# Optimization experiments

Measured on AMD Instinct MI355X. Metric: run time of the kernel, lower is better.

Reference implementation:

```python
import jax, jax.numpy as jnp
import numpy as np
from jax import lax

DILATIONS = (1, 3, 9, 9, 3, 1)  # six mid blocks after the 1x1 input conv


def bilinear_sample(fm, verts):
    # fm: [B,H,W,C]; verts: [B,N,2] in [-1,1]; axis 0 of verts maps to H, axis 1 to W.
    # Matches jax.scipy.ndimage.map_coordinates(order=1, mode='constant'):
    # each out-of-bounds corner contributes 0.
    B, H, W, C = fm.shape
    scale = jnp.array([H - 1, W - 1], fm.dtype) / 2.0
    coords = (verts + 1.0) * scale  # [B,N,2]
    vy, vx = coords[..., 0], coords[..., 1]
    y0 = jnp.floor(vy)
    x0 = jnp.floor(vx)
    wy = (vy - y0)[..., None]
    wx = (vx - x0)[..., None]
    y0i = y0.astype(jnp.int32)
    x0i = x0.astype(jnp.int32)
    fm_flat = fm.reshape(B, H * W, C)

    def corner(yi, xi):
        valid = (yi >= 0) & (yi < H) & (xi >= 0) & (xi < W)
        idx = jnp.clip(yi, 0, H - 1) * W + jnp.clip(xi, 0, W - 1)  # [B,N]
        vals = jnp.take_along_axis(fm_flat, idx[..., None], axis=1)  # [B,N,C]
        return jnp.where(valid[..., None], vals, jnp.zeros((), fm.dtype))

    return ((1 - wy) * (1 - wx) * corner(y0i, x0i)
            + (1 - wy) * wx * corner(y0i, x0i + 1)
            + wy * (1 - wx) * corner(y0i + 1, x0i)
            + wy * wx * corner(y0i + 1, x0i + 1))


def conv1d(x, w, b, dil):
    # x: [B,N,Cin], w: [K,Cin,Cout]; flax nnx.Conv default: stride 1, SAME padding.
    out = lax.conv_general_dilated(x, w, (1,), 'SAME', rhs_dilation=(dil,),
                                   dimension_numbers=('NWC', 'WIO', 'NWC'))
    return out if b is None else out + b


def setup_inputs() -> dict:
    key = jax.random.key(0)
    ks = jax.random.split(key, 8)
    B, N, H, W, Cf, Ch = 16, 1024, 256, 256, 126, 512
    D = Cf + 2
    vertices = jax.random.uniform(ks[0], (B, N, 2), jnp.float32, -1.0, 1.0)
    feature_map = jax.random.normal(ks[1], (B, H, W, Cf), jnp.float32)
    w0 = jax.random.normal(ks[2], (1, D, Ch), jnp.float32) / np.float32(np.sqrt(D))
    b0 = jnp.zeros((Ch,), jnp.float32)
    ws = jax.random.normal(ks[3], (6, 3, Ch, Ch), jnp.float32) / np.float32(np.sqrt(3 * Ch))
    bs = jnp.zeros((6, Ch), jnp.float32)
    w_off = jax.random.normal(ks[4], (1, Ch, 2), jnp.float32) / np.float32(np.sqrt(Ch))
    return {"vertices": vertices, "feature_map": feature_map,
            "w0": w0, "b0": b0, "ws": ws, "bs": bs, "w_off": w_off}


def reference(vertices, feature_map, w0, b0, ws, bs, w_off):
    feat = bilinear_sample(feature_map, vertices)          # [B,N,Cf]
    x = jnp.concatenate([feat, vertices], axis=-1)         # [B,N,Cf+2]
    x = jax.nn.relu(conv1d(x, w0, b0, 1))                  # 1x1 input conv
    for i, dil in enumerate(DILATIONS):                    # fixed 6-layer stack
        x = jax.nn.relu(conv1d(x, ws[i], bs[i], dil))
    return conv1d(x, w_off, None, 1)                       # [B,N,2] offsets
```

## Files before the change

kernel.cpp:

```cpp
#include <hip/hip_runtime.h>

typedef __attribute__((ext_vector_type(4))) float f32x4;
typedef __attribute__((ext_vector_type(8))) _Float16 f16x8;

#define BM 128
#define BK 64

#define OFF_W0T 0
#define OFF_WT  131072
#define OFF_X0  (OFF_WT + 6*512*1536*2)
#define OFF_Y0  (OFF_X0 + 16384*128*2)
#define OFF_Y1  (OFF_Y0 + 16*1056*512*2)

__device__ __forceinline__ void load_lds16(const void* g, void* s) {
    __builtin_amdgcn_global_load_lds(
        (const __attribute__((address_space(1))) void*)g,
        (__attribute__((address_space(3))) void*)s, 16, 0, 0);
}

template<int N> struct IC { static constexpr int v = N; };

__global__ __launch_bounds__(256)
void wprep(const float* __restrict__ ws, const float* __restrict__ w0,
           _Float16* __restrict__ wt, _Float16* __restrict__ w0t)
{
    __shared__ float t[64][65];
    const int tid = threadIdx.x;
    const int tr = tid >> 6;
    const int tc = tid & 63;
    const int z = blockIdx.z;
    if (z < 18) {
        const int l = z / 3, tp = z % 3;
        const float* src = ws + (size_t)z * 512 * 512;
        const int ci0 = blockIdx.y * 64, co0 = blockIdx.x * 64;
        #pragma unroll
        for (int i = 0; i < 16; ++i) { int r = i*4 + tr; t[r][tc] = src[(ci0 + r)*512 + co0 + tc]; }
        __syncthreads();
        _Float16* dst = wt + (size_t)l * 512 * 1536;
        #pragma unroll
        for (int i = 0; i < 16; ++i) { int r = i*4 + tr; dst[(co0 + r)*1536 + tp*512 + ci0 + tc] = (_Float16)t[tc][r]; }
    } else {
        if (blockIdx.y >= 2) return;
        const int ci0 = blockIdx.y * 64, co0 = blockIdx.x * 64;
        #pragma unroll
        for (int i = 0; i < 16; ++i) { int r = i*4 + tr; t[r][tc] = w0[(ci0 + r)*512 + co0 + tc]; }
        __syncthreads();
        #pragma unroll
        for (int i = 0; i < 16; ++i) { int r = i*4 + tr; w0t[(co0 + r)*128 + ci0 + tc] = (_Float16)t[tc][r]; }
    }
}

__global__ __launch_bounds__(256)
void sample_pad_kernel(const float* __restrict__ verts, const float* __restrict__ fm,
                       _Float16* __restrict__ X0, _Float16* __restrict__ Y0,
                       _Float16* __restrict__ Y1)
{
    if (blockIdx.x < 1024) {
        const int i = blockIdx.x * 256 + threadIdx.x;
        const unsigned c2   = i & 255;
        const unsigned t2   = ((unsigned)i) >> 8;
        const unsigned prow = t2 & 31;
        const unsigned b    = (t2 >> 5) & 15;
        const unsigned buf  = t2 >> 9;
        const unsigned row  = prow < 16 ? prow : (1024 + prow);
        unsigned* p = (unsigned*)(buf ? Y1 : Y0);
        p[((size_t)b * 1056 + row) * 256 + c2] = 0u;
        return;
    }
    const int p = (blockIdx.x - 1024) * 4 + (threadIdx.x >> 6);
    const int lane = threadIdx.x & 63;
    const int b = p >> 10;
    const float vy = verts[p*2], vx = verts[p*2 + 1];
    const float cy = (vy + 1.f) * 127.5f;
    const float cx = (vx + 1.f) * 127.5f;
    const float fy = floorf(cy), fx = floorf(cx);
    const int y0 = (int)fy, x0 = (int)fx;
    const float wy = cy - fy, wx = cx - fx;
    float w00 = (1.f - wy) * (1.f - wx), w01 = (1.f - wy) * wx;
    float w10 = wy * (1.f - wx),         w11 = wy * wx;
    const bool vy0 = (unsigned)y0 < 256u, vy1 = (unsigned)(y0 + 1) < 256u;
    const bool vx0 = (unsigned)x0 < 256u, vx1 = (unsigned)(x0 + 1) < 256u;
    w00 = (vy0 && vx0) ? w00 : 0.f;
    w01 = (vy0 && vx1) ? w01 : 0.f;
    w10 = (vy1 && vx0) ? w10 : 0.f;
    w11 = (vy1 && vx1) ? w11 : 0.f;
    const int yc0 = min(max(y0, 0), 255), yc1 = min(max(y0 + 1, 0), 255);
    const int xc0 = min(max(x0, 0), 255), xc1 = min(max(x0 + 1, 0), 255);
    const float* base = fm + (size_t)b * (256 * 256 * 126);
    const float* p00 = base + (yc0 * 256 + xc0) * 126;
    const float* p01 = base + (yc0 * 256 + xc1) * 126;
    const float* p10 = base + (yc1 * 256 + xc0) * 126;
    const float* p11 = base + (yc1 * 256 + xc1) * 126;
    _Float16* xr = X0 + (size_t)p * 128;
    for (int c = lane; c < 126; c += 64) {
        float a = w00 * p00[c] + w01 * p01[c] + w10 * p10[c] + w11 * p11[c];
        xr[c] = (_Float16)a;
    }
    if (lane < 2) xr[126 + lane] = (_Float16)(lane ? vx : vy);
}

__global__ __launch_bounds__(256, 2)
void conv_gemm0(const _Float16* __restrict__ A, const _Float16* __restrict__ WT,
                const float* __restrict__ bias, _Float16* __restrict__ Out)
{
    __shared__ _Float16 Ald[2][128 * 64];
    __shared__ _Float16 Bld[2][128 * 64];
    const int tid  = threadIdx.x;
    const int wid  = tid >> 6;
    const int lane = tid & 63;
    const int wm   = wid >> 1, wn = wid & 1;
    const int b    = blockIdx.x >> 3;
    const int n0   = (blockIdx.x & 7) * 128;
    const int co0  = blockIdx.y * 128;

    const _Float16* Ab = A + ((size_t)b * 1024 + n0) * 128;

    const int srow = lane >> 3;
    const int scol = (((lane & 7) ^ (lane >> 3)) << 3);

    f32x4 acc[4][4] = {};

    #pragma unroll
    for (int ks = 0; ks < 2; ++ks) {
        #pragma unroll
        for (int c = 0; c < 4; ++c) {
            const int grow = 8 * (wid + 4 * c) + srow;
            load_lds16(Ab + (size_t)grow * 128 + ks * 64 + scol, &Ald[ks][(8 * (wid + 4 * c)) * 64]);
        }
        #pragma unroll
        for (int c = 0; c < 4; ++c) {
            const int grow = 8 * (wid + 4 * c) + srow;
            load_lds16(WT + (size_t)(co0 + grow) * 128 + ks * 64 + scol, &Bld[ks][(8 * (wid + 4 * c)) * 64]);
        }
    }

    #pragma unroll
    for (int ks = 0; ks < 2; ++ks) {
        __builtin_amdgcn_sched_barrier(0);
        if (ks == 0) asm volatile("s_waitcnt vmcnt(8)" ::: "memory");
        else         asm volatile("s_waitcnt vmcnt(0)" ::: "memory");
        __builtin_amdgcn_s_barrier();
        __builtin_amdgcn_sched_barrier(0);

        f16x8 af[4][2], bfr[4][2];
        #pragma unroll
        for (int f = 0; f < 4; ++f) {
            const int arow = wm * 64 + f * 16 + (lane & 15);
            const int brow = wn * 64 + f * 16 + (lane & 15);
            #pragma unroll
            for (int kf = 0; kf < 2; ++kf) {
                af[f][kf]  = *(const f16x8*)&Ald[ks][arow * 64 + ((kf * 4 + (lane >> 4)) ^ (arow & 7)) * 8];
                bfr[f][kf] = *(const f16x8*)&Bld[ks][brow * 64 + ((kf * 4 + (lane >> 4)) ^ (brow & 7)) * 8];
            }
        }
        #pragma unroll
        for (int m = 0; m < 4; ++m)
            #pragma unroll
            for (int n = 0; n < 4; ++n)
                #pragma unroll
                for (int kf = 0; kf < 2; ++kf)
                    acc[m][n] = __builtin_amdgcn_mfma_f32_16x16x32_f16(af[m][kf], bfr[n][kf], acc[m][n], 0, 0, 0);
    }

    _Float16* Ob = Out + (size_t)b * (1056 * 512) + (size_t)n0 * 512;
    #pragma unroll
    for (int n = 0; n < 4; ++n) {
        const int co = co0 + wn * 64 + n * 16 + (lane & 15);
        const float bv = bias[co];
        #pragma unroll
        for (int m = 0; m < 4; ++m) {
            #pragma unroll
            for (int j = 0; j < 4; ++j) {
                const int row = wm * 64 + m * 16 + (lane >> 4) * 4 + j;
                float v = acc[m][n][j] + bv;
                v = fmaxf(v, 0.f);
                Ob[(size_t)row * 512 + co] = (_Float16)v;
            }
        }
    }
}

#define ACH_ELEMS (320 * 64)
#define BBUF_ELEMS (128 * 64)
__global__ __launch_bounds__(512, 2)
void conv_gemm8(const _Float16* __restrict__ A, const _Float16* __restrict__ WT,
                const float* __restrict__ bias, _Float16* __restrict__ Out, int dil)
{
    extern __shared__ _Float16 smem[];
    _Float16* Ald = smem;
    _Float16* Bld = smem + 2 * ACH_ELEMS;

    const int tid  = threadIdx.x;
    const int wid  = tid >> 6;
    const int lane = tid & 63;
    const int wm   = wid >> 1;
    const int wn   = wid & 1;

    const int orig = blockIdx.x;
    const int swz  = (orig & 7) * 32 + (orig >> 3);
    const int nblk = swz & 3;
    const int mblk = swz >> 2;
    const int b     = mblk >> 2;
    const int n0row = (mblk & 3) * 256;
    const int co0   = nblk * 128;

    const _Float16* Ab = A + (size_t)b * (1056 * 512) + (size_t)n0row * 512;

    const int srow = lane >> 3;
    const int scol = (((lane & 7) ^ (lane >> 3)) << 3);

    f32x4 acc[4][4] = {};

    auto stageA1 = [&](int cn, int i) {
        const int rb = 8 * (wid + 8 * i);
        const _Float16* src = Ab + (long)(rb + srow - 32) * 512 + cn * 64 + scol;
        load_lds16(src, Ald + (cn & 1) * ACH_ELEMS + rb * 64);
    };
    auto stageB1 = [&](int c2, int t2, int cc) {
        const int grow = 64 * cc + 8 * wid + srow;
        const _Float16* src = WT + (size_t)(co0 + grow) * 1536 + (t2 * 512 + c2 * 64) + scol;
        load_lds16(src, Bld + t2 * BBUF_ELEMS + (64 * cc + 8 * wid) * 64);
    };

    stageA1(0, 0); stageA1(0, 1); stageA1(0, 2); stageA1(0, 3); stageA1(0, 4);
    stageB1(0, 0, 0); stageB1(0, 0, 1);
    stageB1(0, 1, 0); stageB1(0, 1, 1);

    auto body = [&](auto TAPc, auto DOAc, int c) {
        constexpr int TAP = decltype(TAPc)::v;
        constexpr int DOA = decltype(DOAc)::v;

        __builtin_amdgcn_sched_barrier(0);
        if constexpr (TAP == 1 && DOA)       asm volatile("s_waitcnt vmcnt(7)" ::: "memory");
        else if constexpr (TAP == 2 && !DOA) asm volatile("s_waitcnt vmcnt(0)" ::: "memory");
        else                                 asm volatile("s_waitcnt vmcnt(2)" ::: "memory");
        __builtin_amdgcn_s_barrier();
        __builtin_amdgcn_sched_barrier(0);

        const _Float16* Abuf = Ald + (c & 1) * ACH_ELEMS;
        const _Float16* Bbuf = Bld + TAP * BBUF_ELEMS;
        const int shift = (TAP - 1) * dil;
        const int rbase = 32 + wm * 64 + (lane & 15) + shift;
        const int akey  = rbase & 7;
        const int bkey  = lane & 7;

        f16x8 bfr[4][2], af[4][2];
        #pragma unroll
        for (int nf = 0; nf < 4; ++nf) {
            const int row = wn * 64 + nf * 16 + (lane & 15);
            #pragma unroll
            for (int kf = 0; kf < 2; ++kf) {
                const int slot = (kf * 4 + (lane >> 4)) ^ bkey;
                bfr[nf][kf] = *(const f16x8*)&Bbuf[row * 64 + slot * 8];
            }
        }
        #pragma unroll
        for (int kf = 0; kf < 2; ++kf) {
            const int slot = (kf * 4 + (lane >> 4)) ^ akey;
            af[0][kf] = *(const f16x8*)&Abuf[rbase * 64 + slot * 8];
        }
        #pragma unroll
        for (int nf = 0; nf < 4; ++nf)
            #pragma unroll
            for (int kf = 0; kf < 2; ++kf)
                acc[0][nf] = __builtin_amdgcn_mfma_f32_16x16x32_f16(af[0][kf], bfr[nf][kf], acc[0][nf], 0, 0, 0);
        #pragma unroll
        for (int kf = 0; kf < 2; ++kf) {
            const int slot = (kf * 4 + (lane >> 4)) ^ akey;
            af[1][kf] = *(const f16x8*)&Abuf[(rbase + 16) * 64 + slot * 8];
        }
        if constexpr (TAP == 0 && DOA) {
            stageA1(c + 1, 0); stageA1(c + 1, 1); stageA1(c + 1, 2); stageA1(c + 1, 3);
        } else if constexpr (TAP == 0) {
            stageB1(7, 2, 0);
        } else if constexpr (DOA) {
            if constexpr (TAP == 1) stageB1(c + 1, 0, 0);
            else                    stageB1(c + 1, 1, 0);
        }
        #pragma unroll
        for (int nf = 0; nf < 4; ++nf)
            #pragma unroll
            for (int kf = 0; kf < 2; ++kf)
                acc[1][nf] = __builtin_amdgcn_mfma_f32_16x16x32_f16(af[1][kf], bfr[nf][kf], acc[1][nf], 0, 0, 0);
        #pragma unroll
        for (int kf = 0; kf < 2; ++kf) {
            const int slot = (kf * 4 + (lane >> 4)) ^ akey;
            af[2][kf] = *(const f16x8*)&Abuf[(rbase + 32) * 64 + slot * 8];
        }
        if constexpr (TAP == 0 && DOA) {
            stageA1(c + 1, 4);
            stageB1(c, 2, 0); stageB1(c, 2, 1);
        } else if constexpr (TAP == 0) {
            stageB1(7, 2, 1);
        } else if constexpr (DOA) {
            if constexpr (TAP == 1) stageB1(c + 1, 0, 1);
            else                    stageB1(c + 1, 1, 1);
        }
        #pragma unroll
        for (int nf = 0; nf < 4; ++nf)
            #pragma unroll
            for (int kf = 0; kf < 2; ++kf)
                acc[2][nf] = __builtin_amdgcn_mfma_f32_16x16x32_f16(af[2][kf], bfr[nf][kf], acc[2][nf], 0, 0, 0);
        #pragma unroll
        for (int kf = 0; kf < 2; ++kf) {
            const int slot = (kf * 4 + (lane >> 4)) ^ akey;
            af[3][kf] = *(const f16x8*)&Abuf[(rbase + 48) * 64 + slot * 8];
        }
        #pragma unroll
        for (int nf = 0; nf < 4; ++nf)
            #pragma unroll
            for (int kf = 0; kf < 2; ++kf)
                acc[3][nf] = __builtin_amdgcn_mfma_f32_16x16x32_f16(af[3][kf], bfr[nf][kf], acc[3][nf], 0, 0, 0);

        if constexpr (DOA) {
            if constexpr (TAP == 0) {
                __builtin_amdgcn_sched_group_barrier(0x100, 10, 0);
                __builtin_amdgcn_sched_group_barrier(0x008,  8, 0);
                __builtin_amdgcn_sched_group_barrier(0x100,  2, 0);
                __builtin_amdgcn_sched_group_barrier(0x070,  4, 0);
                __builtin_amdgcn_sched_group_barrier(0x008,  8, 0);
                __builtin_amdgcn_sched_group_barrier(0x100,  2, 0);
                __builtin_amdgcn_sched_group_barrier(0x070,  3, 0);
                __builtin_amdgcn_sched_group_barrier(0x008,  8, 0);
                __builtin_amdgcn_sched_group_barrier(0x100,  2, 0);
                __builtin_amdgcn_sched_group_barrier(0x008,  8, 0);
            } else {
                __builtin_amdgcn_sched_group_barrier(0x100, 10, 0);
                __builtin_amdgcn_sched_group_barrier(0x008,  8, 0);
                __builtin_amdgcn_sched_group_barrier(0x100,  2, 0);
                __builtin_amdgcn_sched_group_barrier(0x070,  1, 0);
                __builtin_amdgcn_sched_group_barrier(0x008,  8, 0);
                __builtin_amdgcn_sched_group_barrier(0x100,  2, 0);
                __builtin_amdgcn_sched_group_barrier(0x070,  1, 0);
                __builtin_amdgcn_sched_group_barrier(0x008,  8, 0);
                __builtin_amdgcn_sched_group_barrier(0x100,  2, 0);
                __builtin_amdgcn_sched_group_barrier(0x008,  8, 0);
            }
        }
    };

    #pragma unroll 1
    for (int c = 0; c < 7; ++c) {
        body(IC<0>{}, IC<1>{}, c);
        body(IC<1>{}, IC<1>{}, c);
        body(IC<2>{}, IC<1>{}, c);
    }
    body(IC<0>{}, IC<0>{}, 7);
    body(IC<1>{}, IC<0>{}, 7);
    body(IC<2>{}, IC<0>{}, 7);

    _Float16* Ob = Out + (size_t)b * (1056 * 512) + (size_t)n0row * 512;
    #pragma unroll
    for (int nf = 0; nf < 4; ++nf) {
        const int co = co0 + wn * 64 + nf * 16 + (lane & 15);
        const float bv = bias[co];
        #pragma unroll
        for (int m = 0; m < 4; ++m) {
            #pragma unroll
            for (int j = 0; j < 4; ++j) {
                const int row = wm * 64 + m * 16 + (lane >> 4) * 4 + j;
                float v = acc[m][nf][j] + bv;
                v = fmaxf(v, 0.f);
                Ob[(size_t)row * 512 + co] = (_Float16)v;
            }
        }
    }
}

__global__ __launch_bounds__(256)
void final_conv(const _Float16* __restrict__ Y, const float* __restrict__ woff,
                float* __restrict__ out)
{
    const int r = blockIdx.x * 4 + (threadIdx.x >> 6);
    const int lane = threadIdx.x & 63;
    const int b = r >> 10, n = r & 1023;
    const _Float16* yp = Y + ((size_t)b * 1056 + n) * 512 + lane * 8;
    f16x8 yv = *(const f16x8*)yp;
    const int ci0 = lane * 8;
    float s0 = 0.f, s1 = 0.f;
    #pragma unroll
    for (int e = 0; e < 8; ++e) {
        float y = (float)yv[e];
        s0 += y * woff[(ci0 + e) * 2 + 0];
        s1 += y * woff[(ci0 + e) * 2 + 1];
    }
    #pragma unroll
    for (int off = 32; off; off >>= 1) {
        s0 += __shfl_down(s0, off);
        s1 += __shfl_down(s1, off);
    }
    if (lane == 0) { out[r*2] = s0; out[r*2 + 1] = s1; }
}

extern "C" void kernel_launch(void* const* d_in, const int* in_sizes, int n_in,
                              void* d_out, int out_size, void* d_ws, size_t ws_size,
                              hipStream_t stream)
{
    const float* verts = (const float*)d_in[0];
    const float* fm    = (const float*)d_in[1];
    const float* w0    = (const float*)d_in[2];
    const float* b0    = (const float*)d_in[3];
    const float* ws    = (const float*)d_in[4];
    const float* bs    = (const float*)d_in[5];
    const float* woff  = (const float*)d_in[6];
    float* out = (float*)d_out;

    char* wsp = (char*)d_ws;
    _Float16* W0T = (_Float16*)(wsp + OFF_W0T);
    _Float16* WT  = (_Float16*)(wsp + OFF_WT);
    _Float16* X0  = (_Float16*)(wsp + OFF_X0);
    _Float16* Y0  = (_Float16*)(wsp + OFF_Y0);
    _Float16* Y1  = (_Float16*)(wsp + OFF_Y1);
    _Float16* Y0i = Y0 + 16 * 512;
    _Float16* Y1i = Y1 + 16 * 512;

    hipFuncSetAttribute(reinterpret_cast<const void*>(&conv_gemm8),
                        hipFuncAttributeMaxDynamicSharedMemorySize, 131072);

    wprep<<<dim3(8, 8, 19), 256, 0, stream>>>(ws, w0, WT, W0T);
    sample_pad_kernel<<<5120, 256, 0, stream>>>(verts, fm, X0, Y0, Y1);

    conv_gemm0<<<dim3(128, 4), 256, 0, stream>>>(X0, W0T, b0, Y0i);

    const int DIL[6] = {1, 3, 9, 9, 3, 1};
    _Float16* bufs[2] = {Y0i, Y1i};
    for (int l = 0; l < 6; ++l) {
        conv_gemm8<<<256, 512, 131072, stream>>>(
            bufs[l & 1],
            WT + (size_t)l * 512 * 1536, bs + (size_t)l * 512,
            bufs[(l + 1) & 1], DIL[l]);
    }

    final_conv<<<4096, 256, 0, stream>>>(bufs[0], woff, out);
}
```

Baseline: 176.1 us.

## Fuse final offset conv into last GEMM epilogue and merge prep kernels

Merges the weight-transpose and sampling/padding kernels into a single prep launch, which also zeroes the output buffer. The final 1x1 offset conv is folded into the last dilated-conv GEMM's epilogue. Each block reduces its 128 output channels with shuffles and atomically adds partial sums to the output. This removes two launches and the write and reread of the last activation buffer, at the cost of float atomics (nondeterministic summation order) and a more complex epilogue.

After: 170.1 us. 3.4% less time.

```diff
diff --git a/kernel.cpp b/kernel.cpp
--- a/kernel.cpp
+++ b/kernel.cpp
@@ -2,9 +2,6 @@
 
 typedef __attribute__((ext_vector_type(4))) float f32x4;
 typedef __attribute__((ext_vector_type(8))) _Float16 f16x8;
-
-#define BM 128
-#define BK 64
 
 #define OFF_W0T 0
 #define OFF_WT  131072
@@ -21,42 +18,45 @@
 template<int N> struct IC { static constexpr int v = N; };
 
 __global__ __launch_bounds__(256)
-void wprep(const float* __restrict__ ws, const float* __restrict__ w0,
-           _Float16* __restrict__ wt, _Float16* __restrict__ w0t)
+void prep(const float* __restrict__ ws, const float* __restrict__ w0,
+          _Float16* __restrict__ wt, _Float16* __restrict__ w0t,
+          const float* __restrict__ verts, const float* __restrict__ fm,
+          _Float16* __restrict__ X0, _Float16* __restrict__ Y0,
+          _Float16* __restrict__ Y1, float* __restrict__ outp)
 {
     __shared__ float t[64][65];
+    const int bid = blockIdx.x;
     const int tid = threadIdx.x;
-    const int tr = tid >> 6;
-    const int tc = tid & 63;
-    const int z = blockIdx.z;
-    if (z < 18) {
-        const int l = z / 3, tp = z % 3;
-        const float* src = ws + (size_t)z * 512 * 512;
-        const int ci0 = blockIdx.y * 64, co0 = blockIdx.x * 64;
-        #pragma unroll
-        for (int i = 0; i < 16; ++i) { int r = i*4 + tr; t[r][tc] = src[(ci0 + r)*512 + co0 + tc]; }
-        __syncthreads();
-        _Float16* dst = wt + (size_t)l * 512 * 1536;
-        #pragma unroll
-        for (int i = 0; i < 16; ++i) { int r = i*4 + tr; dst[(co0 + r)*1536 + tp*512 + ci0 + tc] = (_Float16)t[tc][r]; }
-    } else {
-        if (blockIdx.y >= 2) return;
-        const int ci0 = blockIdx.y * 64, co0 = blockIdx.x * 64;
-        #pragma unroll
-        for (int i = 0; i < 16; ++i) { int r = i*4 + tr; t[r][tc] = w0[(ci0 + r)*512 + co0 + tc]; }
-        __syncthreads();
-        #pragma unroll
-        for (int i = 0; i < 16; ++i) { int r = i*4 + tr; w0t[(co0 + r)*128 + ci0 + tc] = (_Float16)t[tc][r]; }
-    }
-}
-
-__global__ __launch_bounds__(256)
-void sample_pad_kernel(const float* __restrict__ verts, const float* __restrict__ fm,
-                       _Float16* __restrict__ X0, _Float16* __restrict__ Y0,
-                       _Float16* __restrict__ Y1)
-{
-    if (blockIdx.x < 1024) {
-        const int i = blockIdx.x * 256 + threadIdx.x;
+    if (bid < 1216) {
+        const int z   = bid >> 6;
+        const int rem = bid & 63;
+        const int bx  = rem & 7;
+        const int by  = rem >> 3;
+        const int tr = tid >> 6;
+        const int tc = tid & 63;
+        if (z < 18) {
+            const int l = z / 3, tp = z % 3;
+            const float* src = ws + (size_t)z * 512 * 512;
+            const int ci0 = by * 64, co0 = bx * 64;
+            #pragma unroll
+            for (int i = 0; i < 16; ++i) { int r = i*4 + tr; t[r][tc] = src[(ci0 + r)*512 + co0 + tc]; }
+            __syncthreads();
+            _Float16* dst = wt + (size_t)l * 512 * 1536;
+            #pragma unroll
+            for (int i = 0; i < 16; ++i) { int r = i*4 + tr; dst[(co0 + r)*1536 + tp*512 + ci0 + tc] = (_Float16)t[tc][r]; }
+        } else {
+            if (by >= 2) return;
+            const int ci0 = by * 64, co0 = bx * 64;
+            #pragma unroll
+            for (int i = 0; i < 16; ++i) { int r = i*4 + tr; t[r][tc] = w0[(ci0 + r)*512 + co0 + tc]; }
+            __syncthreads();
+            #pragma unroll
+            for (int i = 0; i < 16; ++i) { int r = i*4 + tr; w0t[(co0 + r)*128 + ci0 + tc] = (_Float16)t[tc][r]; }
+        }
+        return;
+    }
+    if (bid < 2240) {
+        const int i = (bid - 1216) * 256 + tid;
         const unsigned c2   = i & 255;
         const unsigned t2   = ((unsigned)i) >> 8;
         const unsigned prow = t2 & 31;
@@ -67,8 +67,13 @@
         p[((size_t)b * 1056 + row) * 256 + c2] = 0u;
         return;
     }
-    const int p = (blockIdx.x - 1024) * 4 + (threadIdx.x >> 6);
-    const int lane = threadIdx.x & 63;
+    if (bid < 2272) {
+        const int i = (bid - 2240) * 256 + tid;
+        *(f32x4*)&outp[i * 4] = f32x4{0.f, 0.f, 0.f, 0.f};
+        return;
+    }
+    const int p = (bid - 2272) * 4 + (tid >> 6);
+    const int lane = tid & 63;
     const int b = p >> 10;
     const float vy = verts[p*2], vx = verts[p*2 + 1];
     const float cy = (vy + 1.f) * 127.5f;
@@ -182,9 +187,11 @@
 
 #define ACH_ELEMS (320 * 64)
 #define BBUF_ELEMS (128 * 64)
+template<int FUSE>
 __global__ __launch_bounds__(512, 2)
 void conv_gemm8(const _Float16* __restrict__ A, const _Float16* __restrict__ WT,
-                const float* __restrict__ bias, _Float16* __restrict__ Out, int dil)
+                const float* __restrict__ bias, _Float16* __restrict__ Out, int dil,
+                const float* __restrict__ woff, float* __restrict__ outp)
 {
     extern __shared__ _Float16 smem[];
     _Float16* Ald = smem;
@@ -349,47 +356,55 @@
     body(IC<1>{}, IC<0>{}, 7);
     body(IC<2>{}, IC<0>{}, 7);
 
-    _Float16* Ob = Out + (size_t)b * (1056 * 512) + (size_t)n0row * 512;
+    float bv[4], w0v[4], w1v[4];
     #pragma unroll
     for (int nf = 0; nf < 4; ++nf) {
         const int co = co0 + wn * 64 + nf * 16 + (lane & 15);
-        const float bv = bias[co];
+        bv[nf] = bias[co];
+        if constexpr (FUSE) { w0v[nf] = woff[co * 2 + 0]; w1v[nf] = woff[co * 2 + 1]; }
+    }
+    if constexpr (FUSE) {
         #pragma unroll
         for (int m = 0; m < 4; ++m) {
             #pragma unroll
             for (int j = 0; j < 4; ++j) {
-                const int row = wm * 64 + m * 16 + (lane >> 4) * 4 + j;
-                float v = acc[m][nf][j] + bv;
-                v = fmaxf(v, 0.f);
-                Ob[(size_t)row * 512 + co] = (_Float16)v;
-            }
-        }
-    }
-}
-
-__global__ __launch_bounds__(256)
-void final_conv(const _Float16* __restrict__ Y, const float* __restrict__ woff,
-                float* __restrict__ out)
-{
-    const int r = blockIdx.x * 4 + (threadIdx.x >> 6);
-    const int lane = threadIdx.x & 63;
-    const int b = r >> 10, n = r & 1023;
-    const _Float16* yp = Y + ((size_t)b * 1056 + n) * 512 + lane * 8;
-    f16x8 yv = *(const f16x8*)yp;
-    const int ci0 = lane * 8;
-    float s0 = 0.f, s1 = 0.f;
-    #pragma unroll
-    for (int e = 0; e < 8; ++e) {
-        float y = (float)yv[e];
-        s0 += y * woff[(ci0 + e) * 2 + 0];
-        s1 += y * woff[(ci0 + e) * 2 + 1];
-    }
-    #pragma unroll
-    for (int off = 32; off; off >>= 1) {
-        s0 += __shfl_down(s0, off);
-        s1 += __shfl_down(s1, off);
-    }
-    if (lane == 0) { out[r*2] = s0; out[r*2 + 1] = s1; }
+                float s0 = 0.f, s1 = 0.f;
+                #pragma unroll
+                for (int nf = 0; nf < 4; ++nf) {
+                    float v = fmaxf(acc[m][nf][j] + bv[nf], 0.f);
+                    float vf = (float)(_Float16)v;
+                    s0 += vf * w0v[nf];
+                    s1 += vf * w1v[nf];
+                }
+                #pragma unroll
+                for (int off = 1; off < 16; off <<= 1) {
+                    s0 += __shfl_xor(s0, off);
+                    s1 += __shfl_xor(s1, off);
+                }
+                if ((lane & 15) == 0) {
+                    const int r = b * 1024 + n0row + wm * 64 + m * 16 + (lane >> 4) * 4 + j;
+                    atomicAdd(&outp[r * 2 + 0], s0);
+                    atomicAdd(&outp[r * 2 + 1], s1);
+                }
+            }
+        }
+    } else {
+        _Float16* Ob = Out + (size_t)b * (1056 * 512) + (size_t)n0row * 512;
+        #pragma unroll
+        for (int nf = 0; nf < 4; ++nf) {
+            const int co = co0 + wn * 64 + nf * 16 + (lane & 15);
+            #pragma unroll
+            for (int m = 0; m < 4; ++m) {
+                #pragma unroll
+                for (int j = 0; j < 4; ++j) {
+                    const int row = wm * 64 + m * 16 + (lane >> 4) * 4 + j;
+                    float v = acc[m][nf][j] + bv[nf];
+                    v = fmaxf(v, 0.f);
+                    Ob[(size_t)row * 512 + co] = (_Float16)v;
+                }
+            }
+        }
+    }
 }
 
 extern "C" void kernel_launch(void* const* d_in, const int* in_sizes, int n_in,
@@ -414,22 +429,25 @@
     _Float16* Y0i = Y0 + 16 * 512;
     _Float16* Y1i = Y1 + 16 * 512;
 
-    hipFuncSetAttribute(reinterpret_cast<const void*>(&conv_gemm8),
+    hipFuncSetAttribute(reinterpret_cast<const void*>(&conv_gemm8<0>),
                         hipFuncAttributeMaxDynamicSharedMemorySize, 131072);
-
-    wprep<<<dim3(8, 8, 19), 256, 0, stream>>>(ws, w0, WT, W0T);
-    sample_pad_kernel<<<5120, 256, 0, stream>>>(verts, fm, X0, Y0, Y1);
+    hipFuncSetAttribute(reinterpret_cast<const void*>(&conv_gemm8<1>),
+                        hipFuncAttributeMaxDynamicSharedMemorySize, 131072);
+
+    prep<<<6368, 256, 0, stream>>>(ws, w0, WT, W0T, verts, fm, X0, Y0, Y1, out);
 
     conv_gemm0<<<dim3(128, 4), 256, 0, stream>>>(X0, W0T, b0, Y0i);
 
     const int DIL[6] = {1, 3, 9, 9, 3, 1};
     _Float16* bufs[2] = {Y0i, Y1i};
-    for (int l = 0; l < 6; ++l) {
-        conv_gemm8<<<256, 512, 131072, stream>>>(
+    for (int l = 0; l < 5; ++l) {
+        conv_gemm8<0><<<256, 512, 131072, stream>>>(
             bufs[l & 1],
             WT + (size_t)l * 512 * 1536, bs + (size_t)l * 512,
-            bufs[(l + 1) & 1], DIL[l]);
-    }
-
-    final_conv<<<4096, 256, 0, stream>>>(bufs[0], woff, out);
+            bufs[(l + 1) & 1], DIL[l], woff, out);
+    }
+    conv_gemm8<1><<<256, 512, 131072, stream>>>(
+        bufs[1],
+        WT + (size_t)5 * 512 * 1536, bs + (size_t)5 * 512,
+        bufs[0], DIL[5], woff, out);
 }
```
